# Kernel tuning notes

Measured on AMD Instinct MI355X. Metric: run time of the kernel, lower is better.

## Reference

```python
import jax, jax.numpy as jnp
import numpy as np

B, C, D, H, W = 2, 64, 8, 24, 24  # hidden_dim = C; N = D*H*W = 4608 tokens


def setup_inputs() -> dict:
    key = jax.random.key(0)
    ks = jax.random.split(key, 8)
    s = 1.0 / np.sqrt(C)  # fan-in style init for 1x1 conv weights
    return {
        "x": jax.random.normal(ks[0], (B, C, D, H, W), dtype=jnp.float32),
        "h": jax.random.normal(ks[1], (B, C, D, H, W), dtype=jnp.float32),
        "Wq": jax.random.normal(ks[2], (C, C), dtype=jnp.float32) * s,
        "bq": jax.random.normal(ks[3], (C,), dtype=jnp.float32) * s,
        "Wk": jax.random.normal(ks[4], (C, C), dtype=jnp.float32) * s,
        "bk": jax.random.normal(ks[5], (C,), dtype=jnp.float32) * s,
        "Wv": jax.random.normal(ks[6], (C, C), dtype=jnp.float32) * s,
        "bv": jax.random.normal(ks[7], (C,), dtype=jnp.float32) * s,
    }


def reference(x, h, Wq, bq, Wk, bk, Wv, bv):
    # 1x1 Conv3d == per-token linear over channels
    def proj(inp, Wt, bt):
        f = inp.reshape(inp.shape[0], inp.shape[1], -1)  # [B, C, N]
        return jnp.einsum('oc,bcn->bon', Wt, f) + bt[None, :, None]

    q = proj(x, Wq, bq)  # [B, C, N]
    k = proj(h, Wk, bk)  # [B, C, N]
    v = proj(h, Wv, bv)  # [B, C, N]

    scale = 1.0 / np.sqrt(k.shape[1])  # k.size(1) ** 0.5 == sqrt(C)
    scores = jnp.einsum('bcm,bcn->bmn', q, k) * scale  # [B, N, N]
    attn = jax.nn.softmax(scores, axis=-1)
    out = jnp.einsum('bcn,bmn->bcm', v, attn)  # [B, C, N]
    return out.reshape(h.shape)
```

## Files before the change

kernel.cpp:

```cpp
#include <hip/hip_runtime.h>
#include <hip/hip_bf16.h>

#define C_DIM 64
#define N_TOK 4608
#define NBLK  72
#define B_SZ  2
#define M64BLKS 72
#define NSEG  8
#define SEGLEN (N_TOK / NSEG)
#define KTILES 288
#define VTILES 72
#define OSTR  68

typedef __bf16 bf16x8 __attribute__((ext_vector_type(8)));
typedef float  f32x4  __attribute__((ext_vector_type(4)));


__device__ __forceinline__ void gemm_tile(
    const __hip_bfloat16* wmat, const bf16x8 bin[2], const float* bias,
    int col, int quad, f32x4 acc[4])
{
    #pragma unroll
    for (int ot = 0; ot < 4; ot++) {
        f32x4 a = (f32x4){0.f, 0.f, 0.f, 0.f};
        #pragma unroll
        for (int kh = 0; kh < 2; kh++) {
            bf16x8 wf = *(const bf16x8*)(wmat + (ot * 16 + col) * 72 +
                                         kh * 32 + quad * 8);
            a = __builtin_amdgcn_mfma_f32_16x16x32_bf16(wf, bin[kh], a, 0, 0, 0);
        }
        float4 b4 = *(const float4*)(bias + ot * 16 + quad * 4);
        a[0] += b4.x; a[1] += b4.y; a[2] += b4.z; a[3] += b4.w;
        acc[ot] = a;
    }
}

__global__ __launch_bounds__(256) void proj_kernel(
    const float* __restrict__ x,  const float* __restrict__ h,
    const float* __restrict__ Wq, const float* __restrict__ bq,
    const float* __restrict__ Wk, const float* __restrict__ bk,
    const float* __restrict__ Wv, const float* __restrict__ bv,
    __hip_bfloat16* __restrict__ qS, __hip_bfloat16* __restrict__ kS,
    __hip_bfloat16* __restrict__ vS)
{
    __shared__ __hip_bfloat16 wl[3 * 64 * 72];
    __shared__ __hip_bfloat16 xt[64 * 72];
    __shared__ __hip_bfloat16 ht[64 * 72];
    __shared__ __hip_bfloat16 vl[64 * 72];

    const int b  = blockIdx.x / NBLK;
    const int n0 = (blockIdx.x % NBLK) * 64;
    const int t  = threadIdx.x;

    #pragma unroll
    for (int mat = 0; mat < 3; mat++) {
        const float* W = (mat == 0) ? Wq : ((mat == 1) ? Wk : Wv);
        __hip_bfloat16* wd = wl + mat * (64 * 72);
        #pragma unroll
        for (int i = 0; i < 4; i++) {
            const int ch = i * 256 + t;
            const int o = ch >> 4, c0 = (ch & 15) * 4;
            float4 w4 = *(const float4*)(W + ch * 4);
            union { __hip_bfloat16 e[4]; uint2 v; } pk;
            pk.e[0] = __float2bfloat16(w4.x); pk.e[1] = __float2bfloat16(w4.y);
            pk.e[2] = __float2bfloat16(w4.z); pk.e[3] = __float2bfloat16(w4.w);
            *(uint2*)(wd + o * 72 + c0) = pk.v;
        }
    }
    #pragma unroll
    for (int i = 0; i < 4; i++) {
        const int ch = i * 256 + t;
        const int c = ch >> 4, n4 = (ch & 15) * 4;
        float4 x4 = *(const float4*)(x + (size_t)(b * C_DIM + c) * N_TOK + n0 + n4);
        float4 h4 = *(const float4*)(h + (size_t)(b * C_DIM + c) * N_TOK + n0 + n4);
        xt[(n4 + 0) * 72 + c] = __float2bfloat16(x4.x);
        xt[(n4 + 1) * 72 + c] = __float2bfloat16(x4.y);
        xt[(n4 + 2) * 72 + c] = __float2bfloat16(x4.z);
        xt[(n4 + 3) * 72 + c] = __float2bfloat16(x4.w);
        ht[(n4 + 0) * 72 + c] = __float2bfloat16(h4.x);
        ht[(n4 + 1) * 72 + c] = __float2bfloat16(h4.y);
        ht[(n4 + 2) * 72 + c] = __float2bfloat16(h4.z);
        ht[(n4 + 3) * 72 + c] = __float2bfloat16(h4.w);
    }
    __syncthreads();

    const int wave = t >> 6, lane = t & 63;
    const int col = lane & 15, quad = lane >> 4;

    bf16x8 xb[2], hb[2];
    #pragma unroll
    for (int kh = 0; kh < 2; kh++) {
        xb[kh] = *(const bf16x8*)(xt + (wave * 16 + col) * 72 + kh * 32 + quad * 8);
        hb[kh] = *(const bf16x8*)(ht + (wave * 16 + col) * 72 + kh * 32 + quad * 8);
    }

    f32x4 acc[4];

    gemm_tile(wl + 0 * (64 * 72), xb, bq, col, quad, acc);
    {
        const size_t tile16 = (size_t)b * KTILES + (n0 >> 4) + wave;
        const float SC = 0.125f * 1.44269504088896f;
        #pragma unroll
        for (int ot = 0; ot < 4; ot++) {
            union { __hip_bfloat16 e[4]; uint2 v; } pk;
            #pragma unroll
            for (int r = 0; r < 4; r++) pk.e[r] = __float2bfloat16(acc[ot][r] * SC);
            *(uint2*)(qS + (tile16 << 10) + (ot >> 1) * 512 +
                      ((ot * 2 + (quad >> 1)) & 3) * 128 + col * 8 +
                      (quad & 1) * 4) = pk.v;
        }
    }

    gemm_tile(wl + 1 * (64 * 72), hb, bk, col, quad, acc);
    {
        const int t_l = (wave >> 1) * 2 + ((col >> 2) & 1);
        const int row = ((wave * 2 + (col >> 3)) & 3) * 4 + (col & 3);
        const size_t tile16 = (size_t)b * KTILES + (n0 >> 4) + t_l;
        #pragma unroll
        for (int ot = 0; ot < 4; ot++) {
            union { __hip_bfloat16 e[4]; uint2 v; } pk;
            #pragma unroll
            for (int r = 0; r < 4; r++) pk.e[r] = __float2bfloat16(acc[ot][r]);
            *(uint2*)(kS + (tile16 << 10) + (ot >> 1) * 512 +
                      ((ot * 2 + (quad >> 1)) & 3) * 128 + row * 8 +
                      (quad & 1) * 4) = pk.v;
        }
    }

    gemm_tile(wl + 2 * (64 * 72), hb, bv, col, quad, acc);
    #pragma unroll
    for (int ot = 0; ot < 4; ot++)
        #pragma unroll
        for (int r = 0; r < 4; r++)
            vl[(ot * 16 + quad * 4 + r) * 72 + wave * 16 + col] =
                __float2bfloat16(acc[ot][r]);
    __syncthreads();
    {
        const size_t vbase = ((size_t)(b * VTILES) + (n0 >> 6)) << 12;
        #pragma unroll
        for (int rep = 0; rep < 2; rep++) {
            const int ch = rep * 256 + t;
            const int cc = ch >> 7, hf = (ch >> 6) & 1;
            const int qd = (ch >> 4) & 3, c2 = ch & 15;
            *(uint4*)(vS + vbase + (size_t)ch * 8) =
                *(const uint4*)(vl + (cc * 16 + c2) * 72 + hf * 32 + qd * 8);
        }
    }
}

__global__ __launch_bounds__(512) void attn_kernel(
    const __hip_bfloat16* __restrict__ qS,
    const __hip_bfloat16* __restrict__ kS,
    const __hip_bfloat16* __restrict__ vS,
    float* __restrict__ out)
{
    __shared__ float o_lds[NSEG * 16 * OSTR];
    __shared__ float lstat[NSEG][64];

    const int b    = blockIdx.x / M64BLKS;
    const int mblk = blockIdx.x % M64BLKS;
    const int wave = threadIdx.x >> 6;
    const int lane = threadIdx.x & 63;
    const int col  = lane & 15;
    const int quad = lane >> 4;
    const int m0   = mblk * 64;

    const __hip_bfloat16* qp =
        qS + (((size_t)b * KTILES + (m0 >> 4)) << 10) + lane * 8;
    bf16x8 qa[4][2];
    #pragma unroll
    for (int ms = 0; ms < 4; ms++) {
        qa[ms][0] = *(const bf16x8*)(qp + ms * 1024);
        qa[ms][1] = *(const bf16x8*)(qp + ms * 1024 + 512);
    }

    f32x4 accO[4][4];
    #pragma unroll
    for (int ms = 0; ms < 4; ms++)
        #pragma unroll
        for (int cc = 0; cc < 4; cc++)
            accO[ms][cc] = (f32x4){0.f, 0.f, 0.f, 0.f};
    float rsum[4] = {0.f, 0.f, 0.f, 0.f};

    const int nbeg = wave * SEGLEN;

    #pragma unroll 1
    for (int n0 = nbeg; n0 < nbeg + SEGLEN; n0 += 64) {
        const __hip_bfloat16* kt =
            kS + (((size_t)b * KTILES + (n0 >> 4)) << 10) + lane * 8;
        bf16x8 ka[8];
        #pragma unroll
        for (int j = 0; j < 4; j++) {
            ka[2 * j]     = *(const bf16x8*)(kt + (j << 10));
            ka[2 * j + 1] = *(const bf16x8*)(kt + (j << 10) + 512);
        }
        const __hip_bfloat16* vt =
            vS + ((((size_t)b * VTILES) + (n0 >> 6)) << 12) + lane * 8;
        bf16x8 va[8];
        #pragma unroll
        for (int cc = 0; cc < 4; cc++) {
            va[2 * cc]     = *(const bf16x8*)(vt + cc * 1024);
            va[2 * cc + 1] = *(const bf16x8*)(vt + cc * 1024 + 512);
        }

        #pragma unroll
        for (int ms = 0; ms < 4; ms++) {
            f32x4 s[4];
            #pragma unroll
            for (int j = 0; j < 4; j++) {
                s[j] = __builtin_amdgcn_mfma_f32_16x16x32_bf16(
                           ka[2 * j], qa[ms][0], (f32x4){0.f, 0.f, 0.f, 0.f}, 0, 0, 0);
                s[j] = __builtin_amdgcn_mfma_f32_16x16x32_bf16(
                           ka[2 * j + 1], qa[ms][1], s[j], 0, 0, 0);
            }
            union { __hip_bfloat16 e[8]; bf16x8 v; } p0, p1;
            float ps = 0.f;
            #pragma unroll
            for (int j = 0; j < 2; j++)
                #pragma unroll
                for (int r = 0; r < 4; r++) {
                    float e0 = __builtin_amdgcn_exp2f(s[j][r]);
                    float e1 = __builtin_amdgcn_exp2f(s[2 + j][r]);
                    ps += e0 + e1;
                    p0.e[j * 4 + r] = __float2bfloat16(e0);
                    p1.e[j * 4 + r] = __float2bfloat16(e1);
                }
            rsum[ms] += ps;
            #pragma unroll
            for (int cc = 0; cc < 4; cc++) {
                accO[ms][cc] = __builtin_amdgcn_mfma_f32_16x16x32_bf16(
                                   va[2 * cc], p0.v, accO[ms][cc], 0, 0, 0);
                accO[ms][cc] = __builtin_amdgcn_mfma_f32_16x16x32_bf16(
                                   va[2 * cc + 1], p1.v, accO[ms][cc], 0, 0, 0);
            }
        }
    }

    #pragma unroll
    for (int ms = 0; ms < 4; ms++) {
        rsum[ms] += __shfl_xor(rsum[ms], 16);
        rsum[ms] += __shfl_xor(rsum[ms], 32);
    }
    if (quad == 0) {
        #pragma unroll
        for (int ms = 0; ms < 4; ms++) lstat[wave][ms * 16 + col] = rsum[ms];
    }

    #pragma unroll
    for (int phase = 0; phase < 4; phase++) {
        #pragma unroll
        for (int cc = 0; cc < 4; cc++)
            *(f32x4*)(o_lds + (wave * 16 + col) * OSTR + cc * 16 + quad * 4) =
                accO[phase][cc];
        __syncthreads();
        if (threadIdx.x < 256) {
            const int m  = threadIdx.x & 15;
            const int cq = threadIdx.x >> 4;
            const int mi = phase * 16 + m;
            float lsum = 0.f;
            f32x4 oacc = (f32x4){0.f, 0.f, 0.f, 0.f};
            #pragma unroll
            for (int sgm = 0; sgm < NSEG; sgm++) {
                lsum += lstat[sgm][mi];
                oacc += *(const f32x4*)(o_lds + (sgm * 16 + m) * OSTR + cq * 4);
            }
            const float inv = 1.0f / lsum;
            #pragma unroll
            for (int r = 0; r < 4; r++) {
                const int c = cq * 4 + r;
                out[(size_t)(b * C_DIM + c) * N_TOK + m0 + phase * 16 + m] =
                    oacc[r] * inv;
            }
        }
        __syncthreads();
    }
}

extern "C" void kernel_launch(void* const* d_in, const int* in_sizes, int n_in,
                              void* d_out, int out_size, void* d_ws, size_t ws_size,
                              hipStream_t stream) {
    const float* x  = (const float*)d_in[0];
    const float* h  = (const float*)d_in[1];
    const float* Wq = (const float*)d_in[2];
    const float* bq = (const float*)d_in[3];
    const float* Wk = (const float*)d_in[4];
    const float* bk = (const float*)d_in[5];
    const float* Wv = (const float*)d_in[6];
    const float* bv = (const float*)d_in[7];
    float* out = (float*)d_out;

    const size_t elems = (size_t)B_SZ * N_TOK * C_DIM;
    __hip_bfloat16* qS = (__hip_bfloat16*)d_ws;
    __hip_bfloat16* kS = qS + elems;
    __hip_bfloat16* vS = kS + elems;

    proj_kernel<<<B_SZ * NBLK, 256, 0, stream>>>(x, h, Wq, bq, Wk, bk, Wv, bv,
                                                 qS, kS, vS);
    attn_kernel<<<B_SZ * M64BLKS, 512, 0, stream>>>(qS, kS, vS, out);
}
```

Baseline: 93.52 us.

## Split projection across waves per matrix and halve token tile

The projection kernel now processes 32-token tiles with 384 threads, giving each pair of waves one of the Q/K/V matrices instead of every wave computing all three serially. Weights are read straight from global memory and converted to bf16 in registers, so the shared-memory weight staging and its barrier go away. This doubles the block count and shortens per-wave work on a small prologue kernel, in exchange for redundant weight loads across blocks and more complex output indexing into the tiled K/V layouts.

Result: slower. 97.94 us (+4.7%).

```diff
diff --git a/kernel.cpp b/kernel.cpp
--- a/kernel.cpp
+++ b/kernel.cpp
@@ -3,7 +3,7 @@
 
 #define C_DIM 64
 #define N_TOK 4608
-#define NBLK  72
+#define PBLK  144
 #define B_SZ  2
 #define M64BLKS 72
 #define NSEG  8
@@ -16,26 +16,7 @@
 typedef float  f32x4  __attribute__((ext_vector_type(4)));
 
 
-__device__ __forceinline__ void gemm_tile(
-    const __hip_bfloat16* wmat, const bf16x8 bin[2], const float* bias,
-    int col, int quad, f32x4 acc[4])
-{
-    #pragma unroll
-    for (int ot = 0; ot < 4; ot++) {
-        f32x4 a = (f32x4){0.f, 0.f, 0.f, 0.f};
-        #pragma unroll
-        for (int kh = 0; kh < 2; kh++) {
-            bf16x8 wf = *(const bf16x8*)(wmat + (ot * 16 + col) * 72 +
-                                         kh * 32 + quad * 8);
-            a = __builtin_amdgcn_mfma_f32_16x16x32_bf16(wf, bin[kh], a, 0, 0, 0);
-        }
-        float4 b4 = *(const float4*)(bias + ot * 16 + quad * 4);
-        a[0] += b4.x; a[1] += b4.y; a[2] += b4.z; a[3] += b4.w;
-        acc[ot] = a;
-    }
-}
-
-__global__ __launch_bounds__(256) void proj_kernel(
+__global__ __launch_bounds__(384) void proj_kernel(
     const float* __restrict__ x,  const float* __restrict__ h,
     const float* __restrict__ Wq, const float* __restrict__ bq,
     const float* __restrict__ Wk, const float* __restrict__ bk,
@@ -43,62 +24,68 @@
     __hip_bfloat16* __restrict__ qS, __hip_bfloat16* __restrict__ kS,
     __hip_bfloat16* __restrict__ vS)
 {
-    __shared__ __hip_bfloat16 wl[3 * 64 * 72];
-    __shared__ __hip_bfloat16 xt[64 * 72];
-    __shared__ __hip_bfloat16 ht[64 * 72];
-    __shared__ __hip_bfloat16 vl[64 * 72];
-
-    const int b  = blockIdx.x / NBLK;
-    const int n0 = (blockIdx.x % NBLK) * 64;
+    __shared__ __hip_bfloat16 xt[32 * 72];
+    __shared__ __hip_bfloat16 ht[32 * 72];
+    __shared__ __hip_bfloat16 vl[64 * 36];
+
+    const int b  = blockIdx.x / PBLK;
+    const int n0 = (blockIdx.x % PBLK) * 32;
     const int t  = threadIdx.x;
 
-    #pragma unroll
-    for (int mat = 0; mat < 3; mat++) {
-        const float* W = (mat == 0) ? Wq : ((mat == 1) ? Wk : Wv);
-        __hip_bfloat16* wd = wl + mat * (64 * 72);
-        #pragma unroll
-        for (int i = 0; i < 4; i++) {
-            const int ch = i * 256 + t;
-            const int o = ch >> 4, c0 = (ch & 15) * 4;
-            float4 w4 = *(const float4*)(W + ch * 4);
-            union { __hip_bfloat16 e[4]; uint2 v; } pk;
-            pk.e[0] = __float2bfloat16(w4.x); pk.e[1] = __float2bfloat16(w4.y);
-            pk.e[2] = __float2bfloat16(w4.z); pk.e[3] = __float2bfloat16(w4.w);
-            *(uint2*)(wd + o * 72 + c0) = pk.v;
-        }
-    }
-    #pragma unroll
-    for (int i = 0; i < 4; i++) {
-        const int ch = i * 256 + t;
-        const int c = ch >> 4, n4 = (ch & 15) * 4;
-        float4 x4 = *(const float4*)(x + (size_t)(b * C_DIM + c) * N_TOK + n0 + n4);
-        float4 h4 = *(const float4*)(h + (size_t)(b * C_DIM + c) * N_TOK + n0 + n4);
-        xt[(n4 + 0) * 72 + c] = __float2bfloat16(x4.x);
-        xt[(n4 + 1) * 72 + c] = __float2bfloat16(x4.y);
-        xt[(n4 + 2) * 72 + c] = __float2bfloat16(x4.z);
-        xt[(n4 + 3) * 72 + c] = __float2bfloat16(x4.w);
-        ht[(n4 + 0) * 72 + c] = __float2bfloat16(h4.x);
-        ht[(n4 + 1) * 72 + c] = __float2bfloat16(h4.y);
-        ht[(n4 + 2) * 72 + c] = __float2bfloat16(h4.z);
-        ht[(n4 + 3) * 72 + c] = __float2bfloat16(h4.w);
+    for (int ch = t; ch < 1024; ch += 384) {
+        const bool isx = ch < 512;
+        const int  c2  = isx ? ch : ch - 512;
+        const int  c   = c2 >> 3, n4 = (c2 & 7) * 4;
+        const float* src = isx ? x : h;
+        __hip_bfloat16* dst = isx ? xt : ht;
+        float4 v4 = *(const float4*)(src + (size_t)(b * C_DIM + c) * N_TOK + n0 + n4);
+        dst[(n4 + 0) * 72 + c] = __float2bfloat16(v4.x);
+        dst[(n4 + 1) * 72 + c] = __float2bfloat16(v4.y);
+        dst[(n4 + 2) * 72 + c] = __float2bfloat16(v4.z);
+        dst[(n4 + 3) * 72 + c] = __float2bfloat16(v4.w);
     }
     __syncthreads();
 
     const int wave = t >> 6, lane = t & 63;
     const int col = lane & 15, quad = lane >> 4;
-
-    bf16x8 xb[2], hb[2];
-    #pragma unroll
-    for (int kh = 0; kh < 2; kh++) {
-        xb[kh] = *(const bf16x8*)(xt + (wave * 16 + col) * 72 + kh * 32 + quad * 8);
-        hb[kh] = *(const bf16x8*)(ht + (wave * 16 + col) * 72 + kh * 32 + quad * 8);
-    }
+    const int mat = wave >> 1;
+    const int sub = wave & 1;
+
+    const __hip_bfloat16* srcT = (mat == 0) ? xt : ht;
+    bf16x8 bin[2];
+    #pragma unroll
+    for (int kh = 0; kh < 2; kh++)
+        bin[kh] = *(const bf16x8*)(srcT + (sub * 16 + col) * 72 + kh * 32 + quad * 8);
+
+    const float* W    = (mat == 0) ? Wq : ((mat == 1) ? Wk : Wv);
+    const float* bias = (mat == 0) ? bq : ((mat == 1) ? bk : bv);
 
     f32x4 acc[4];
-
-    gemm_tile(wl + 0 * (64 * 72), xb, bq, col, quad, acc);
-    {
-        const size_t tile16 = (size_t)b * KTILES + (n0 >> 4) + wave;
+    #pragma unroll
+    for (int ot = 0; ot < 4; ot++) {
+        f32x4 a = (f32x4){0.f, 0.f, 0.f, 0.f};
+        #pragma unroll
+        for (int kh = 0; kh < 2; kh++) {
+            const float* wp = W + (ot * 16 + col) * 64 + kh * 32 + quad * 8;
+            float4 w0 = *(const float4*)(wp);
+            float4 w1 = *(const float4*)(wp + 4);
+            union { __hip_bfloat16 e[8]; bf16x8 v; } wf;
+            wf.e[0] = __float2bfloat16(w0.x); wf.e[1] = __float2bfloat16(w0.y);
+            wf.e[2] = __float2bfloat16(w0.z); wf.e[3] = __float2bfloat16(w0.w);
+            wf.e[4] = __float2bfloat16(w1.x); wf.e[5] = __float2bfloat16(w1.y);
+            wf.e[6] = __float2bfloat16(w1.z); wf.e[7] = __float2bfloat16(w1.w);
+            a = __builtin_amdgcn_mfma_f32_16x16x32_bf16(wf.v, bin[kh], a, 0, 0, 0);
+        }
+        float4 b4 = *(const float4*)(bias + ot * 16 + quad * 4);
+        a[0] += b4.x; a[1] += b4.y; a[2] += b4.z; a[3] += b4.w;
+        acc[ot] = a;
+    }
+
+    const int half32 = (n0 >> 5) & 1;
+    const int tile64 = n0 >> 6;
+
+    if (mat == 0) {
+        const size_t tile16 = (size_t)b * KTILES + (n0 >> 4) + sub;
         const float SC = 0.125f * 1.44269504088896f;
         #pragma unroll
         for (int ot = 0; ot < 4; ot++) {
@@ -109,13 +96,10 @@
                       ((ot * 2 + (quad >> 1)) & 3) * 128 + col * 8 +
                       (quad & 1) * 4) = pk.v;
         }
-    }
-
-    gemm_tile(wl + 1 * (64 * 72), hb, bk, col, quad, acc);
-    {
-        const int t_l = (wave >> 1) * 2 + ((col >> 2) & 1);
-        const int row = ((wave * 2 + (col >> 3)) & 3) * 4 + (col & 3);
-        const size_t tile16 = (size_t)b * KTILES + (n0 >> 4) + t_l;
+    } else if (mat == 1) {
+        const int t_l = half32 * 2 + ((col >> 2) & 1);
+        const int row = ((sub * 2 + (col >> 3)) & 3) * 4 + (col & 3);
+        const size_t tile16 = (size_t)b * KTILES + tile64 * 4 + t_l;
         #pragma unroll
         for (int ot = 0; ot < 4; ot++) {
             union { __hip_bfloat16 e[4]; uint2 v; } pk;
@@ -125,26 +109,20 @@
                       ((ot * 2 + (quad >> 1)) & 3) * 128 + row * 8 +
                       (quad & 1) * 4) = pk.v;
         }
-    }
-
-    gemm_tile(wl + 2 * (64 * 72), hb, bv, col, quad, acc);
-    #pragma unroll
-    for (int ot = 0; ot < 4; ot++)
-        #pragma unroll
-        for (int r = 0; r < 4; r++)
-            vl[(ot * 16 + quad * 4 + r) * 72 + wave * 16 + col] =
-                __float2bfloat16(acc[ot][r]);
+    } else {
+        #pragma unroll
+        for (int ot = 0; ot < 4; ot++)
+            #pragma unroll
+            for (int r = 0; r < 4; r++)
+                vl[(ot * 16 + quad * 4 + r) * 36 + sub * 16 + col] =
+                    __float2bfloat16(acc[ot][r]);
+    }
     __syncthreads();
-    {
-        const size_t vbase = ((size_t)(b * VTILES) + (n0 >> 6)) << 12;
-        #pragma unroll
-        for (int rep = 0; rep < 2; rep++) {
-            const int ch = rep * 256 + t;
-            const int cc = ch >> 7, hf = (ch >> 6) & 1;
-            const int qd = (ch >> 4) & 3, c2 = ch & 15;
-            *(uint4*)(vS + vbase + (size_t)ch * 8) =
-                *(const uint4*)(vl + (cc * 16 + c2) * 72 + hf * 32 + qd * 8);
-        }
+    if (t < 256) {
+        const int cc = t >> 6, qd = (t >> 4) & 3, c2 = t & 15;
+        *(uint4*)(vS + (((size_t)b * VTILES + tile64) << 12) + cc * 1024 +
+                  half32 * 512 + qd * 128 + c2 * 8) =
+            *(const uint4*)(vl + (cc * 16 + c2) * 36 + qd * 8);
     }
 }
 
@@ -294,7 +272,7 @@
     __hip_bfloat16* kS = qS + elems;
     __hip_bfloat16* vS = kS + elems;
 
-    proj_kernel<<<B_SZ * NBLK, 256, 0, stream>>>(x, h, Wq, bq, Wk, bk, Wv, bv,
+    proj_kernel<<<B_SZ * PBLK, 384, 0, stream>>>(x, h, Wq, bq, Wk, bk, Wv, bv,
                                                  qS, kS, vS);
     attn_kernel<<<B_SZ * M64BLKS, 512, 0, stream>>>(qS, kS, vS, out);
 }
```
